# Performance work log

Measured on AMD Instinct MI355X. Metric: run time of the kernel, lower is better.

## Reference

```python
import jax, jax.numpy as jnp
import numpy as np

N = 100000
E = 3200000


def setup_inputs() -> dict:
    key = jax.random.key(0)
    k1, k2, k3 = jax.random.split(key, 3)
    x = jax.random.normal(k1, (N, 256), dtype=jnp.float32)
    edge_index = jax.random.randint(k2, (2, E), 0, N, dtype=jnp.int64)
    W = jax.random.normal(k3, (256, 64), dtype=jnp.float32) * (1.0 / np.sqrt(256.0))
    b = jnp.zeros((64,), dtype=jnp.float32)
    return {"x": x, "edge_index": edge_index, "W": W, "b": b}


def reference(x, edge_index, W, b):
    # GCNConv (PyG defaults): add self-loops, symmetric deg normalization,
    # linear transform, neighbor aggregation, bias.
    n = x.shape[0]
    loops = jnp.arange(n, dtype=edge_index.dtype)
    row = jnp.concatenate([edge_index[0], loops])  # src
    col = jnp.concatenate([edge_index[1], loops])  # dst

    # degree over destination nodes (incl. self-loops)
    deg = jax.ops.segment_sum(jnp.ones_like(col, dtype=x.dtype), col, num_segments=n)
    deg_inv_sqrt = jnp.where(deg > 0, jax.lax.rsqrt(deg), 0.0)
    norm = deg_inv_sqrt[row] * deg_inv_sqrt[col]  # [E+N]

    h = x @ W  # [N, C]
    msgs = h[row] * norm[:, None]  # gather + scale
    out = jax.ops.segment_sum(msgs, col, num_segments=n)  # scatter-add
    return out + b
```

## Files before the change

### kernel.cpp

```cpp
#include <hip/hip_runtime.h>

#define C_IN 256
#define C_OUT 64
#define BSH 7
#define NPB 128
#define NB 1024
#define CHUNK 4096
#define ROWS 4

typedef short bf16x8 __attribute__((ext_vector_type(8)));
typedef float f32x4 __attribute__((ext_vector_type(4)));

__device__ __forceinline__ unsigned short f2bf(float f) {
    unsigned u = __builtin_bit_cast(unsigned, f);
    u = (u + 0x7FFFu + ((u >> 16) & 1u)) >> 16;
    return (unsigned short)u;
}
__device__ __forceinline__ float bflo(unsigned u) {
    return __builtin_bit_cast(float, u << 16);
}
__device__ __forceinline__ float bfhi(unsigned u) {
    return __builtin_bit_cast(float, u & 0xffff0000u);
}

__global__ __launch_bounds__(256) void k_wt(const float* __restrict__ W,
                                            unsigned short* __restrict__ WTs) {
#pragma unroll
    for (int i = 0; i < 16; ++i) {
        int f = i * 256 + threadIdx.x;
        int k = f >> 4;
        int n4 = (f & 15) * 4;
        float4 v = ((const float4*)W)[f];
        int c = k >> 3, ci = k & 7;
        float vv[4] = {v.x, v.y, v.z, v.w};
#pragma unroll
        for (int r = 0; r < 4; ++r) {
            int row = n4 + r;
            WTs[row * 256 + ((c ^ (row & 7)) << 3) + ci] = f2bf(vv[r]);
        }
    }
}

__global__ __launch_bounds__(1024) void k_hist2(const int* __restrict__ dst,
                                                int* __restrict__ table, int e) {
    __shared__ int cnt[NB];
    if (threadIdx.x < NB) cnt[threadIdx.x] = 0;
    __syncthreads();
    int b0 = blockIdx.x * CHUNK;
#pragma unroll
    for (int k = 0; k < CHUNK / 1024; ++k) {
        int i = b0 + k * 1024 + threadIdx.x;
        if (i < e) atomicAdd(&cnt[dst[i] >> BSH], 1);
    }
    __syncthreads();
    if (threadIdx.x < NB) table[(size_t)blockIdx.x * NB + threadIdx.x] = cnt[threadIdx.x];
}

__global__ __launch_bounds__(256) void kA2(int* __restrict__ table,
                                           int* __restrict__ tot, int nbin) {
    __shared__ int part[256];
    int bucket = blockIdx.x;
    int t = threadIdx.x;
    int v[ROWS];
    int s = 0;
#pragma unroll
    for (int i = 0; i < ROWS; ++i) {
        int r = t * ROWS + i;
        int x = (r < nbin) ? table[(size_t)r * NB + bucket] : 0;
        v[i] = s;
        s += x;
    }
    part[t] = s;
    __syncthreads();
    for (int off = 1; off < 256; off <<= 1) {
        int u = (t >= off) ? part[t - off] : 0;
        __syncthreads();
        part[t] += u;
        __syncthreads();
    }
    int base = part[t] - s;
#pragma unroll
    for (int i = 0; i < ROWS; ++i) {
        int r = t * ROWS + i;
        if (r < nbin) table[(size_t)r * NB + bucket] = v[i] + base;
    }
    if (t == 255) tot[bucket] = part[255];
}

__global__ __launch_bounds__(1024) void kB(const int* __restrict__ tot,
                                           int* __restrict__ gbase, int e) {
    __shared__ int l[NB];
    int t = threadIdx.x;
    int v = tot[t];
    l[t] = v;
    __syncthreads();
    for (int off = 1; off < NB; off <<= 1) {
        int u = (t >= off) ? l[t - off] : 0;
        __syncthreads();
        l[t] += u;
        __syncthreads();
    }
    gbase[t] = l[t] - v;
    if (t == NB - 1) gbase[NB] = e;
}

__global__ __launch_bounds__(1024) void k_bin2(const int* __restrict__ src,
                                               const int* __restrict__ dst,
                                               const int* __restrict__ table,
                                               const int* __restrict__ gbase,
                                               int* __restrict__ sorted, int e) {
    __shared__ int cur[NB];
    if (threadIdx.x < NB)
        cur[threadIdx.x] = table[(size_t)blockIdx.x * NB + threadIdx.x] + gbase[threadIdx.x];
    __syncthreads();
    int b0 = blockIdx.x * CHUNK;
#pragma unroll
    for (int k = 0; k < CHUNK / 1024; ++k) {
        int i = b0 + k * 1024 + threadIdx.x;
        if (i < e) {
            int d = dst[i];
            int bb = d >> BSH;
            int off = atomicAdd(&cur[bb], 1);
            sorted[off] = (src[i] << BSH) | (d & (NPB - 1));
        }
    }
}

__global__ __launch_bounds__(512) void k_sort2(const int* __restrict__ sorted,
                                               const int* __restrict__ gbase,
                                               int* __restrict__ eidx,
                                               int* __restrict__ rowptr,
                                               float* __restrict__ dinv, int n, int e) {
    __shared__ int cnt[NPB];
    __shared__ int sc[NPB];
    __shared__ int cur[NPB];
    int b = blockIdx.x;
    int node0 = b * NPB;
    int range = min(NPB, n - node0);
    int inbase = gbase[b];
    int m_b = gbase[b + 1] - inbase;
    if (threadIdx.x < NPB) cnt[threadIdx.x] = 0;
    __syncthreads();
    for (int j = threadIdx.x; j < m_b; j += 512)
        atomicAdd(&cnt[sorted[inbase + j] & (NPB - 1)], 1);
    __syncthreads();
    if (threadIdx.x < NPB) sc[threadIdx.x] = cnt[threadIdx.x];
    __syncthreads();
    for (int off = 1; off < NPB; off <<= 1) {
        int t = (threadIdx.x < NPB && threadIdx.x >= off) ? sc[threadIdx.x - off] : 0;
        __syncthreads();
        if (threadIdx.x < NPB) sc[threadIdx.x] += t;
        __syncthreads();
    }
    if (threadIdx.x < NPB) {
        int excl = inbase + sc[threadIdx.x] - cnt[threadIdx.x];
        cur[threadIdx.x] = excl;
        if (threadIdx.x < range) {
            rowptr[node0 + threadIdx.x] = excl;
            dinv[node0 + threadIdx.x] = rsqrtf((float)(cnt[threadIdx.x] + 1));
        }
    }
    __syncthreads();
    for (int j = threadIdx.x; j < m_b; j += 512) {
        int v = sorted[inbase + j];
        int pos = atomicAdd(&cur[v & (NPB - 1)], 1);
        eidx[pos] = v >> BSH;
    }
    if (b == 0 && threadIdx.x == 0) rowptr[n] = e;
}

__global__ __launch_bounds__(256, 3) void k_gemm(const float* __restrict__ x,
                                                 const unsigned short* __restrict__ WTs,
                                                 const float* __restrict__ dinv,
                                                 unsigned short* __restrict__ h, int n) {
    __shared__ unsigned short Wl[64 * 256];

    const int t = threadIdx.x;
    const int lane = t & 63;
    const int wv = t >> 6;
    const int m = lane & 15;
    const int q = lane >> 4;
    const int mx = m & 7;

    if (blockIdx.x == 0 && t < 8)
        *(uint4*)&h[(size_t)n * C_OUT + t * 8] = make_uint4(0u, 0u, 0u, 0u);

#pragma unroll
    for (int j = 0; j < 8; ++j) {
        const unsigned short* gsrc = WTs + j * 2048 + wv * 512 + lane * 8;
        unsigned short* ldst = Wl + j * 2048 + wv * 512;
        __builtin_amdgcn_global_load_lds(
            (const __attribute__((address_space(1))) unsigned int*)gsrc,
            (__attribute__((address_space(3))) unsigned int*)ldst, 16, 0, 0);
    }

    int arow = blockIdx.x * 64 + 16 * wv + m;
    const float* xp = x + (size_t)(arow < n ? arow : 0) * C_IN + q * 8;
    float4 raw[16];
#pragma unroll
    for (int ks = 0; ks < 8; ++ks) {
        const float* p0 = xp + ks * 32;
        const float* p1 = xp + ks * 32 + 4;
        asm volatile("global_load_dwordx4 %0, %1, off" : "=v"(raw[2 * ks]) : "v"(p0));
        asm volatile("global_load_dwordx4 %0, %1, off" : "=v"(raw[2 * ks + 1]) : "v"(p1));
    }

    asm volatile("s_waitcnt vmcnt(0)" ::: "memory");
    __builtin_amdgcn_sched_barrier(0);
    __syncthreads();

    float di[4];
#pragma unroll
    for (int r = 0; r < 4; ++r) {
        int gr = blockIdx.x * 64 + 16 * wv + q * 4 + r;
        di[r] = dinv[gr < n ? gr : 0];
    }

    bf16x8 A[8];
#pragma unroll
    for (int ks = 0; ks < 8; ++ks) {
        float4 v0 = raw[2 * ks];
        float4 v1 = raw[2 * ks + 1];
        bf16x8 a;
        a[0] = (short)f2bf(v0.x); a[1] = (short)f2bf(v0.y);
        a[2] = (short)f2bf(v0.z); a[3] = (short)f2bf(v0.w);
        a[4] = (short)f2bf(v1.x); a[5] = (short)f2bf(v1.y);
        a[6] = (short)f2bf(v1.z); a[7] = (short)f2bf(v1.w);
        A[ks] = a;
    }

    f32x4 acc[4];
#pragma unroll
    for (int nt = 0; nt < 4; ++nt) acc[nt] = (f32x4){0.f, 0.f, 0.f, 0.f};

#pragma unroll
    for (int ks = 0; ks < 8; ++ks) {
        int c = ks * 4 + q;
        int cs = (c ^ mx) << 3;
#pragma unroll
        for (int nt = 0; nt < 4; ++nt) {
            bf16x8 B = *(const bf16x8*)&Wl[(nt * 16 + m) * 256 + cs];
            acc[nt] = __builtin_amdgcn_mfma_f32_16x16x32_bf16(A[ks], B, acc[nt], 0, 0, 0);
        }
    }

#pragma unroll
    for (int r = 0; r < 4; ++r) {
        int gr = blockIdx.x * 64 + 16 * wv + q * 4 + r;
        if (gr < n) {
#pragma unroll
            for (int nt = 0; nt < 4; ++nt)
                h[(size_t)gr * C_OUT + nt * 16 + m] = f2bf(acc[nt][r] * di[r]);
        }
    }
}

#define GROUND(T, HV)                                                                   \
    {                                                                                   \
        int s_ = __shfl(eid, (T) * 8 + g, 64);                                          \
        const unsigned short* p_ = h + (size_t)s_ * C_OUT + c8;                         \
        asm volatile("global_load_dwordx4 %0, %1, off" : "=v"(HV) : "v"(p_));           \
    }
#define ACC8(HV)                                                                        \
    {                                                                                   \
        a0 += bflo(HV.x); a1 += bfhi(HV.x); a2 += bflo(HV.y); a3 += bfhi(HV.y);         \
        a4 += bflo(HV.z); a5 += bfhi(HV.z); a6 += bflo(HV.w); a7 += bfhi(HV.w);         \
    }

__global__ __launch_bounds__(256) void k_gather(const int* __restrict__ rowptr,
                                                const int* __restrict__ eidx,
                                                const unsigned short* __restrict__ h,
                                                const float* __restrict__ dinv,
                                                const float* __restrict__ bias,
                                                float* __restrict__ out, int n) {
    int node = blockIdx.x * 4 + (threadIdx.x >> 6);
    if (node >= n) return;
    int lane = threadIdx.x & 63;
    int g = lane >> 3;
    int c8 = (lane & 7) * 8;

    int beg = rowptr[node];
    int end = rowptr[node + 1];
    int cnt = end - beg;

    float a0 = 0.f, a1 = 0.f, a2 = 0.f, a3 = 0.f;
    float a4 = 0.f, a5 = 0.f, a6 = 0.f, a7 = 0.f;

    {
        int idx = beg + lane;
        int eid = (idx < end) ? eidx[idx] : n;
        uint4 hv0, hv1, hv2, hv3, hv4, hv5, hv6, hv7;
        GROUND(0, hv0); GROUND(1, hv1); GROUND(2, hv2); GROUND(3, hv3);
        bool more = cnt > 32;
        if (more) { GROUND(4, hv4); GROUND(5, hv5); GROUND(6, hv6); GROUND(7, hv7); }
        asm volatile("s_waitcnt vmcnt(0)" ::: "memory");
        __builtin_amdgcn_sched_barrier(0);
        ACC8(hv0); ACC8(hv1); ACC8(hv2); ACC8(hv3);
        if (more) { ACC8(hv4); ACC8(hv5); ACC8(hv6); ACC8(hv7); }
    }
    for (int j = beg + 64; j < end; j += 64) {
        int idx = j + lane;
        int eid = (idx < end) ? eidx[idx] : n;
        uint4 hv0, hv1, hv2, hv3, hv4, hv5, hv6, hv7;
        GROUND(0, hv0); GROUND(1, hv1); GROUND(2, hv2); GROUND(3, hv3);
        bool more = (end - j) > 32;
        if (more) { GROUND(4, hv4); GROUND(5, hv5); GROUND(6, hv6); GROUND(7, hv7); }
        asm volatile("s_waitcnt vmcnt(0)" ::: "memory");
        __builtin_amdgcn_sched_barrier(0);
        ACC8(hv0); ACC8(hv1); ACC8(hv2); ACC8(hv3);
        if (more) { ACC8(hv4); ACC8(hv5); ACC8(hv6); ACC8(hv7); }
    }

#pragma unroll
    for (int off = 8; off < 64; off <<= 1) {
        a0 += __shfl_xor(a0, off, 64); a1 += __shfl_xor(a1, off, 64);
        a2 += __shfl_xor(a2, off, 64); a3 += __shfl_xor(a3, off, 64);
        a4 += __shfl_xor(a4, off, 64); a5 += __shfl_xor(a5, off, 64);
        a6 += __shfl_xor(a6, off, 64); a7 += __shfl_xor(a7, off, 64);
    }
    if (g == 0) {
        float di = dinv[node];
        uint4 sv = *(const uint4*)&h[(size_t)node * C_OUT + c8];
        float4 b0 = *(const float4*)&bias[c8];
        float4 b1 = *(const float4*)&bias[c8 + 4];
        float4 o0, o1;
        o0.x = (a0 + bflo(sv.x)) * di + b0.x;
        o0.y = (a1 + bfhi(sv.x)) * di + b0.y;
        o0.z = (a2 + bflo(sv.y)) * di + b0.z;
        o0.w = (a3 + bfhi(sv.y)) * di + b0.w;
        o1.x = (a4 + bflo(sv.z)) * di + b1.x;
        o1.y = (a5 + bfhi(sv.z)) * di + b1.y;
        o1.z = (a6 + bflo(sv.w)) * di + b1.z;
        o1.w = (a7 + bfhi(sv.w)) * di + b1.w;
        *(float4*)&out[(size_t)node * C_OUT + c8] = o0;
        *(float4*)&out[(size_t)node * C_OUT + c8 + 4] = o1;
    }
}

extern "C" void kernel_launch(void* const* d_in, const int* in_sizes, int n_in,
                              void* d_out, int out_size, void* d_ws, size_t ws_size,
                              hipStream_t stream) {
    const float* x = (const float*)d_in[0];
    const int* ei = (const int*)d_in[1];
    const float* W = (const float*)d_in[2];
    const float* bias = (const float*)d_in[3];
    float* out = (float*)d_out;

    const int n = in_sizes[0] / C_IN;
    const int e = in_sizes[1] / 2;
    const int* src = ei;
    const int* dst = ei + e;

    const int nbin = (e + CHUNK - 1) / CHUNK;
    const int nbuck = (n + NPB - 1) / NPB;

    char* w = (char*)d_ws;
    unsigned short* h = (unsigned short*)w;  w += ((size_t)n + 1) * C_OUT * 2;
    int* sorted = (int*)w;                   w += (size_t)e * 4;
    int* eidx = (int*)w;                     w += (size_t)e * 4;
    float* dinv = (float*)w;                 w += (size_t)n * 4;
    int* rowptr = (int*)w;                   w += (size_t)(n + 1) * 4;
    int* table = (int*)w;                    w += (size_t)nbin * NB * 4;
    int* tot = (int*)w;                      w += NB * 4;
    int* gbase = (int*)w;                    w += (NB + 1) * 4;
    unsigned short* WTs = (unsigned short*)w; w += (size_t)C_OUT * C_IN * 2;

    k_wt<<<1, 256, 0, stream>>>(W, WTs);
    k_hist2<<<nbin, 1024, 0, stream>>>(dst, table, e);
    kA2<<<NB, 256, 0, stream>>>(table, tot, nbin);
    kB<<<1, 1024, 0, stream>>>(tot, gbase, e);
    k_bin2<<<nbin, 1024, 0, stream>>>(src, dst, table, gbase, sorted, e);
    k_sort2<<<nbuck, 512, 0, stream>>>(sorted, gbase, eidx, rowptr, dinv, n, e);
    k_gemm<<<(n + 63) / 64, 256, 0, stream>>>(x, WTs, dinv, h, n);
    k_gather<<<(n + 3) / 4, 256, 0, stream>>>(rowptr, eidx, h, dinv, bias, out, n);
}
```

Before: 329.0 us.

## Stage binning in LDS for coalesced scatter, widen chunks, restructure bucket scan

The binning kernel now does a local counting sort of each 8192-edge chunk in shared memory before writing. Edges belonging to the same bucket then go out as contiguous runs instead of scattered single-word stores through global-offset atomics. The chunk size doubles, and the per-bucket column scan now handles 16 buckets per block with 32 rows per thread, giving coalesced table reads. The per-bucket sort kernel stages its edge slice in LDS when it fits, so the second pass avoids re-reading global memory. The cost is heavy LDS use per block (about 52KB in binning), which lowers occupancy, plus an extra block-wide 1024-entry scan.

```diff
diff --git a/kernel.cpp b/kernel.cpp
--- a/kernel.cpp
+++ b/kernel.cpp
@@ -5,8 +5,9 @@
 #define BSH 7
 #define NPB 128
 #define NB 1024
-#define CHUNK 4096
-#define ROWS 4
+#define CHUNK 8192
+#define RG 32
+#define SCAP 6144
 
 typedef short bf16x8 __attribute__((ext_vector_type(8)));
 typedef float f32x4 __attribute__((ext_vector_type(4)));
@@ -44,7 +45,7 @@
 __global__ __launch_bounds__(1024) void k_hist2(const int* __restrict__ dst,
                                                 int* __restrict__ table, int e) {
     __shared__ int cnt[NB];
-    if (threadIdx.x < NB) cnt[threadIdx.x] = 0;
+    cnt[threadIdx.x] = 0;
     __syncthreads();
     int b0 = blockIdx.x * CHUNK;
 #pragma unroll
@@ -53,38 +54,41 @@
         if (i < e) atomicAdd(&cnt[dst[i] >> BSH], 1);
     }
     __syncthreads();
-    if (threadIdx.x < NB) table[(size_t)blockIdx.x * NB + threadIdx.x] = cnt[threadIdx.x];
+    table[(size_t)blockIdx.x * NB + threadIdx.x] = cnt[threadIdx.x];
 }
 
 __global__ __launch_bounds__(256) void kA2(int* __restrict__ table,
                                            int* __restrict__ tot, int nbin) {
     __shared__ int part[256];
-    int bucket = blockIdx.x;
     int t = threadIdx.x;
-    int v[ROWS];
+    int bc = t & 15, rg = t >> 4;
+    int B = blockIdx.x * 16 + bc;
+    int v[RG];
     int s = 0;
 #pragma unroll
-    for (int i = 0; i < ROWS; ++i) {
-        int r = t * ROWS + i;
-        int x = (r < nbin) ? table[(size_t)r * NB + bucket] : 0;
+    for (int i = 0; i < RG; ++i) {
+        int r = rg * RG + i;
+        int x = (r < nbin) ? table[(size_t)r * NB + B] : 0;
         v[i] = s;
         s += x;
     }
     part[t] = s;
     __syncthreads();
-    for (int off = 1; off < 256; off <<= 1) {
-        int u = (t >= off) ? part[t - off] : 0;
+#pragma unroll
+    for (int off = 1; off < 16; off <<= 1) {
+        int u = (rg >= off) ? part[t - off * 16] : 0;
         __syncthreads();
         part[t] += u;
         __syncthreads();
     }
-    int base = part[t] - s;
-#pragma unroll
-    for (int i = 0; i < ROWS; ++i) {
-        int r = t * ROWS + i;
-        if (r < nbin) table[(size_t)r * NB + bucket] = v[i] + base;
-    }
-    if (t == 255) tot[bucket] = part[255];
+    int incl = part[t];
+    int base = incl - s;
+#pragma unroll
+    for (int i = 0; i < RG; ++i) {
+        int r = rg * RG + i;
+        if (r < nbin) table[(size_t)r * NB + B] = base + v[i];
+    }
+    if (rg == 15) tot[B] = incl;
 }
 
 __global__ __launch_bounds__(1024) void kB(const int* __restrict__ tot,
@@ -109,19 +113,59 @@
                                                const int* __restrict__ table,
                                                const int* __restrict__ gbase,
                                                int* __restrict__ sorted, int e) {
-    __shared__ int cur[NB];
-    if (threadIdx.x < NB)
-        cur[threadIdx.x] = table[(size_t)blockIdx.x * NB + threadIdx.x] + gbase[threadIdx.x];
+    __shared__ int stage[CHUNK];
+    __shared__ unsigned short sbkt[CHUNK];
+    __shared__ int lcnt[NB];
+    __shared__ int lsc[NB];
+    __shared__ int lbase[NB];
+    int t = threadIdx.x;
+    lcnt[t] = 0;
     __syncthreads();
     int b0 = blockIdx.x * CHUNK;
+
+    int bb[CHUNK / 1024], pv[CHUNK / 1024], rk[CHUNK / 1024];
 #pragma unroll
     for (int k = 0; k < CHUNK / 1024; ++k) {
-        int i = b0 + k * 1024 + threadIdx.x;
+        int i = b0 + k * 1024 + t;
         if (i < e) {
             int d = dst[i];
-            int bb = d >> BSH;
-            int off = atomicAdd(&cur[bb], 1);
-            sorted[off] = (src[i] << BSH) | (d & (NPB - 1));
+            bb[k] = d >> BSH;
+            pv[k] = (src[i] << BSH) | (d & (NPB - 1));
+            rk[k] = atomicAdd(&lcnt[bb[k]], 1);
+        } else {
+            bb[k] = -1;
+        }
+    }
+    __syncthreads();
+    lsc[t] = lcnt[t];
+    __syncthreads();
+    for (int off = 1; off < NB; off <<= 1) {
+        int u = (t >= off) ? lsc[t - off] : 0;
+        __syncthreads();
+        lsc[t] += u;
+        __syncthreads();
+    }
+    lbase[t] = lsc[t] - lcnt[t];
+    __syncthreads();
+    int tot = lsc[NB - 1];
+
+#pragma unroll
+    for (int k = 0; k < CHUNK / 1024; ++k) {
+        if (bb[k] >= 0) {
+            int p = lbase[bb[k]] + rk[k];
+            stage[p] = pv[k];
+            sbkt[p] = (unsigned short)bb[k];
+        }
+    }
+    lcnt[t] = gbase[t] + table[(size_t)blockIdx.x * NB + t];
+    __syncthreads();
+
+#pragma unroll
+    for (int k = 0; k < CHUNK / 1024; ++k) {
+        int j = k * 1024 + t;
+        if (j < tot) {
+            int B = sbkt[j];
+            sorted[lcnt[B] + (j - lbase[B])] = stage[j];
         }
     }
 }
@@ -134,15 +178,21 @@
     __shared__ int cnt[NPB];
     __shared__ int sc[NPB];
     __shared__ int cur[NPB];
+    __shared__ int sstage[SCAP];
     int b = blockIdx.x;
     int node0 = b * NPB;
     int range = min(NPB, n - node0);
     int inbase = gbase[b];
     int m_b = gbase[b + 1] - inbase;
+    bool fits = (m_b <= SCAP);
     if (threadIdx.x < NPB) cnt[threadIdx.x] = 0;
-    __syncthreads();
-    for (int j = threadIdx.x; j < m_b; j += 512)
-        atomicAdd(&cnt[sorted[inbase + j] & (NPB - 1)], 1);
+    if (fits)
+        for (int j = threadIdx.x; j < m_b; j += 512) sstage[j] = sorted[inbase + j];
+    __syncthreads();
+    for (int j = threadIdx.x; j < m_b; j += 512) {
+        int v = fits ? sstage[j] : sorted[inbase + j];
+        atomicAdd(&cnt[v & (NPB - 1)], 1);
+    }
     __syncthreads();
     if (threadIdx.x < NPB) sc[threadIdx.x] = cnt[threadIdx.x];
     __syncthreads();
@@ -162,7 +212,7 @@
     }
     __syncthreads();
     for (int j = threadIdx.x; j < m_b; j += 512) {
-        int v = sorted[inbase + j];
+        int v = fits ? sstage[j] : sorted[inbase + j];
         int pos = atomicAdd(&cur[v & (NPB - 1)], 1);
         eidx[pos] = v >> BSH;
     }
@@ -367,7 +417,7 @@
 
     k_wt<<<1, 256, 0, stream>>>(W, WTs);
     k_hist2<<<nbin, 1024, 0, stream>>>(dst, table, e);
-    kA2<<<NB, 256, 0, stream>>>(table, tot, nbin);
+    kA2<<<NB / 16, 256, 0, stream>>>(table, tot, nbin);
     kB<<<1, 1024, 0, stream>>>(tot, gbase, e);
     k_bin2<<<nbin, 1024, 0, stream>>>(src, dst, table, gbase, sorted, e);
     k_sort2<<<nbuck, 512, 0, stream>>>(sorted, gbase, eidx, rowptr, dinv, n, e);
```

After: 287.2 us. 1.15x faster.
